# Optimization experiments

Measured on AMD Instinct MI355X. Metric: run time of the kernel, lower is better.

## Reference

```python
import jax, jax.numpy as jnp
import numpy as np

D = 512
H = 8
HD = D // H
S = 2048
B = 4


def setup_inputs() -> dict:
    key = jax.random.key(0)
    ks = jax.random.split(key, 8)
    scale = 1.0 / np.sqrt(D)
    x = jax.random.normal(ks[0], (S, B, D), dtype=jnp.float32)
    head_mask = jax.random.normal(ks[1], (H, S, S), dtype=jnp.float32)
    value_gate = jax.random.uniform(ks[2], (1, B, 1), dtype=jnp.float32)
    # nn.MultiheadAttention parameters
    in_proj_w = jax.random.normal(ks[3], (3 * D, D), dtype=jnp.float32) * scale
    in_proj_b = jnp.zeros((3 * D,), dtype=jnp.float32)
    out_proj_w = jax.random.normal(ks[4], (D, D), dtype=jnp.float32) * scale
    out_proj_b = jnp.zeros((D,), dtype=jnp.float32)
    return {
        "x": x,
        "head_mask": head_mask,
        "value_gate": value_gate,
        "in_proj_w": in_proj_w,
        "in_proj_b": in_proj_b,
        "out_proj_w": out_proj_w,
        "out_proj_b": out_proj_b,
    }


def reference(x, head_mask, value_gate, in_proj_w, in_proj_b, out_proj_w, out_proj_b):
    # x: (S, B, D); head_mask: (H, S, S) additive; value_gate: (1, B, 1)
    v_in = x * value_gate  # value gating before projection
    wq, wk, wv = in_proj_w[:D], in_proj_w[D:2 * D], in_proj_w[2 * D:]
    bq, bk, bv = in_proj_b[:D], in_proj_b[D:2 * D], in_proj_b[2 * D:]
    q = x @ wq.T + bq            # (S, B, D)
    k = x @ wk.T + bk
    v = v_in @ wv.T + bv
    # split D into H heads of size HD (matches torch's view(S, B*H, HD))
    q = q.reshape(S, B, H, HD)
    k = k.reshape(S, B, H, HD)
    v = v.reshape(S, B, H, HD)
    scores = jnp.einsum('sbhd,tbhd->bhst', q, k) / np.sqrt(HD).astype(np.float32)
    scores = scores + head_mask[None]  # broadcast per-head mask over batch
    attn = jax.nn.softmax(scores, axis=-1)  # (B, H, S, S)
    out = jnp.einsum('bhst,tbhd->sbhd', attn, v).reshape(S, B, D)
    return out @ out_proj_w.T + out_proj_b
```

## Files before the change

kernel.cpp:

```cpp
#include <hip/hip_runtime.h>
#include <cstdint>
#include <cstddef>

typedef _Float16 half8 __attribute__((ext_vector_type(8)));
typedef _Float16 half4 __attribute__((ext_vector_type(4)));
typedef float f32x4 __attribute__((ext_vector_type(4)));

#define MFMA16(A,B,C) __builtin_amdgcn_mfma_f32_16x16x32_f16(A,B,C,0,0,0)

__device__ __forceinline__ void gll16(const _Float16* g, _Float16* l) {
    __builtin_amdgcn_global_load_lds(
        (const __attribute__((address_space(1))) void*)g,
        (__attribute__((address_space(3))) void*)l, 16, 0, 0);
}

__global__ __launch_bounds__(256) void cvt_f16(
    const float* __restrict__ X, const float* __restrict__ Wi, const float* __restrict__ Wo,
    _Float16* __restrict__ Xh, _Float16* __restrict__ Wih, _Float16* __restrict__ Woh)
{
    const size_t i8 = ((size_t)blockIdx.x * 256 + threadIdx.x) * 8;
    const size_t NX = (size_t)4194304, NWI = 786432;
    const float* src; _Float16* dst; size_t off;
    if (i8 < NX) { src = X; dst = Xh; off = i8; }
    else if (i8 < NX + NWI) { src = Wi; dst = Wih; off = i8 - NX; }
    else { src = Wo; dst = Woh; off = i8 - NX - NWI; }
    f32x4 v0 = *(const f32x4*)(src + off);
    f32x4 v1 = *(const f32x4*)(src + off + 4);
    half8 r;
    r[0]=(_Float16)v0[0]; r[1]=(_Float16)v0[1]; r[2]=(_Float16)v0[2]; r[3]=(_Float16)v0[3];
    r[4]=(_Float16)v1[0]; r[5]=(_Float16)v1[1]; r[6]=(_Float16)v1[2]; r[7]=(_Float16)v1[3];
    *(half8*)(dst + off) = r;
}

__global__ __launch_bounds__(256) void qkv_mfma(
    const _Float16* __restrict__ X, const _Float16* __restrict__ W,
    const float* __restrict__ bias, const float* __restrict__ gate,
    _Float16* __restrict__ Qo, _Float16* __restrict__ Ko, _Float16* __restrict__ Vt)
{
    __shared__ _Float16 As[128][72];
    __shared__ _Float16 Bs[64][72];
    const int tid = threadIdx.x;
    const int lane = tid & 63, wv = tid >> 6;
    const int l15 = lane & 15, g = lane >> 4;
    const int wr = wv >> 1, wc = wv & 1;
    const int j0 = blockIdx.x * 64, r0 = blockIdx.y * 128;
    f32x4 acc[4][2] = {};
    const int arow = tid >> 1, ahf = tid & 1;
    const int brow = tid >> 2, bc = tid & 3;
    for (int k0 = 0; k0 < 512; k0 += 64) {
        const _Float16* srca = X + (size_t)(r0 + arow) * 512 + k0 + ahf * 32;
#pragma unroll
        for (int c = 0; c < 4; ++c)
            *(half8*)&As[arow][ahf * 32 + c * 8] = *(const half8*)(srca + c * 8);
        const _Float16* srcb = W + (size_t)(j0 + brow) * 512 + k0 + bc * 16;
#pragma unroll
        for (int c = 0; c < 2; ++c)
            *(half8*)&Bs[brow][bc * 16 + c * 8] = *(const half8*)(srcb + c * 8);
        __syncthreads();
#pragma unroll
        for (int kt = 0; kt < 2; ++kt) {
            half8 bf0 = *(half8*)&Bs[32 * wc + l15][kt * 32 + g * 8];
            half8 bf1 = *(half8*)&Bs[32 * wc + 16 + l15][kt * 32 + g * 8];
#pragma unroll
            for (int ri = 0; ri < 4; ++ri) {
                half8 af = *(half8*)&As[64 * wr + 16 * ri + l15][kt * 32 + g * 8];
                acc[ri][0] = MFMA16(af, bf0, acc[ri][0]);
                acc[ri][1] = MFMA16(af, bf1, acc[ri][1]);
            }
        }
        __syncthreads();
    }
#pragma unroll
    for (int ri = 0; ri < 4; ++ri) {
#pragma unroll
        for (int cj = 0; cj < 2; ++cj) {
            const int col = j0 + 32 * wc + 16 * cj + l15;
            const int sec = col >> 9, hh = (col >> 6) & 7, d = col & 63;
            const float bv = bias[col];
#pragma unroll
            for (int r = 0; r < 4; ++r) {
                const int row = r0 + 64 * wr + 16 * ri + 4 * g + r;
                const int b = row & 3, s = row >> 2;
                const float v = acc[ri][cj][r];
                if (sec == 0)
                    Qo[((size_t)(b * 8 + hh) * 2048 + s) * 64 + d] = (_Float16)((v + bv) * 0.125f);
                else if (sec == 1)
                    Ko[((size_t)(b * 8 + hh) * 2048 + s) * 64 + d] = (_Float16)(v + bv);
                else {
                    const int ps = (s & ~31) | ((s & 12) << 1) | ((s & 16) >> 2) | (s & 3);
                    Vt[((size_t)(b * 8 + hh) * 64 + d) * 2048 + ps] = (_Float16)(v * gate[b] + bv);
                }
            }
        }
    }
}

__global__ __launch_bounds__(128, 2) void attn_mfma(
    const _Float16* __restrict__ Q, const _Float16* __restrict__ K,
    const _Float16* __restrict__ V, const float* __restrict__ M,
    _Float16* __restrict__ P0, _Float16* __restrict__ P1, float* __restrict__ Lb)
{
    __shared__ _Float16 Kl[2][4096];
    __shared__ _Float16 Vl[2][4096];
    const int tid = threadIdx.x;
    const int lane = tid & 63, w = tid >> 6;
    const int l15 = lane & 15, g = lane >> 4;
    const int bsw = l15 & 7;
    const int bid = blockIdx.x;
    const int h = bid & 7, b = (bid >> 3) & 3, sg = (bid >> 5) & 15, kvh = bid >> 9;
    const int s0 = sg * 128 + w * 64;
    const size_t bh = (size_t)b * 8 + h;
    const _Float16* Qp = Q + bh * 2048 * 64;
    const _Float16* Kp = K + bh * 2048 * 64 + (size_t)kvh * 1024 * 64;
    const _Float16* Vp = V + bh * 64 * 2048 + kvh * 1024;
    const float* Mp = M + (size_t)h * 2048 * 2048 + kvh * 1024;

    half8 qf[4][2];
#pragma unroll
    for (int qj = 0; qj < 4; ++qj)
#pragma unroll
        for (int dh = 0; dh < 2; ++dh)
            qf[qj][dh] = *(const half8*)(Qp + (size_t)(s0 + 16 * qj + l15) * 64 + dh * 32 + g * 8);

    const int grow = lane >> 3, gcb = lane & 7;

    if (w == 0) {
#pragma unroll
        for (int c = 0; c < 8; ++c) {
            const int r = c * 8 + grow;
            gll16(Kp + (size_t)r * 64 + ((gcb ^ (r & 7)) * 8), &Kl[0][c * 512]);
        }
    } else {
#pragma unroll
        for (int c = 0; c < 8; ++c) {
            const int d = c * 8 + grow;
            gll16(Vp + (size_t)d * 2048 + ((gcb ^ (d & 7)) * 8), &Vl[0][c * 512]);
        }
    }
    f32x4 mc0[2][4], mc1[2][4];
#pragma unroll
    for (int mi = 0; mi < 2; ++mi)
#pragma unroll
        for (int qj = 0; qj < 4; ++qj)
            mc0[mi][qj] = *(const f32x4*)(Mp + (size_t)(s0 + 16 * qj + l15) * 2048 + 16 * mi + 4 * g);

    f32x4 O[4][4] = {};
    float l[4] = {0.f, 0.f, 0.f, 0.f};
    __syncthreads();

    for (int tl = 0; tl < 16; ++tl) {
        const int cur = tl & 1;
        const int t0 = tl * 64;
        const int tn = ((tl + 1) & 15) * 64;
        if (tl < 15) {
            if (w == 0) {
#pragma unroll
                for (int c = 0; c < 8; ++c) {
                    const int r = c * 8 + grow;
                    gll16(Kp + (size_t)(t0 + 64 + r) * 64 + ((gcb ^ (r & 7)) * 8),
                          &Kl[cur ^ 1][c * 512]);
                }
            } else {
#pragma unroll
                for (int c = 0; c < 8; ++c) {
                    const int d = c * 8 + grow;
                    gll16(Vp + (size_t)d * 2048 + t0 + 64 + ((gcb ^ (d & 7)) * 8),
                          &Vl[cur ^ 1][c * 512]);
                }
            }
        }

        f32x4 St[2][4];
        __builtin_amdgcn_s_setprio(1);
#pragma unroll
        for (int mi = 0; mi < 2; ++mi) {
            const int row = 16 * mi + l15;
            half8 kf0 = *(half8*)&Kl[cur][row * 64 + ((g) ^ bsw) * 8];
            half8 kf1 = *(half8*)&Kl[cur][row * 64 + ((4 + g) ^ bsw) * 8];
#pragma unroll
            for (int qj = 0; qj < 4; ++qj) {
                St[mi][qj] = MFMA16(kf0, qf[qj][0], mc0[mi][qj]);
                St[mi][qj] = MFMA16(kf1, qf[qj][1], St[mi][qj]);
            }
        }
        __builtin_amdgcn_s_setprio(0);
#pragma unroll
        for (int mi = 0; mi < 2; ++mi)
#pragma unroll
            for (int qj = 0; qj < 4; ++qj)
                mc1[mi][qj] = *(const f32x4*)(Mp + (size_t)(s0 + 16 * qj + l15) * 2048 + t0 + 16 * (2 + mi) + 4 * g);
        half8 pfA[4];
#pragma unroll
        for (int qj = 0; qj < 4; ++qj) {
            float e00 = __expf(St[0][qj][0]), e01 = __expf(St[0][qj][1]);
            float e02 = __expf(St[0][qj][2]), e03 = __expf(St[0][qj][3]);
            float e10 = __expf(St[1][qj][0]), e11 = __expf(St[1][qj][1]);
            float e12 = __expf(St[1][qj][2]), e13 = __expf(St[1][qj][3]);
            l[qj] += ((e00 + e01) + (e02 + e03)) + ((e10 + e11) + (e12 + e13));
            half8 p;
            p[0] = (_Float16)e00; p[1] = (_Float16)e01; p[2] = (_Float16)e02; p[3] = (_Float16)e03;
            p[4] = (_Float16)e10; p[5] = (_Float16)e11; p[6] = (_Float16)e12; p[7] = (_Float16)e13;
            pfA[qj] = p;
        }
        __builtin_amdgcn_s_setprio(1);
#pragma unroll
        for (int di = 0; di < 4; ++di) {
            const int vrow = 16 * di + l15;
            half8 vf = *(half8*)&Vl[cur][vrow * 64 + ((g) ^ bsw) * 8];
#pragma unroll
            for (int qj = 0; qj < 4; ++qj)
                O[di][qj] = MFMA16(vf, pfA[qj], O[di][qj]);
        }
        __builtin_amdgcn_s_setprio(0);

        __builtin_amdgcn_s_setprio(1);
#pragma unroll
        for (int mi = 0; mi < 2; ++mi) {
            const int row = 16 * (2 + mi) + l15;
            half8 kf0 = *(half8*)&Kl[cur][row * 64 + ((g) ^ bsw) * 8];
            half8 kf1 = *(half8*)&Kl[cur][row * 64 + ((4 + g) ^ bsw) * 8];
#pragma unroll
            for (int qj = 0; qj < 4; ++qj) {
                St[mi][qj] = MFMA16(kf0, qf[qj][0], mc1[mi][qj]);
                St[mi][qj] = MFMA16(kf1, qf[qj][1], St[mi][qj]);
            }
        }
        __builtin_amdgcn_s_setprio(0);
#pragma unroll
        for (int mi = 0; mi < 2; ++mi)
#pragma unroll
            for (int qj = 0; qj < 4; ++qj)
                mc0[mi][qj] = *(const f32x4*)(Mp + (size_t)(s0 + 16 * qj + l15) * 2048 + tn + 16 * mi + 4 * g);
        half8 pfB[4];
#pragma unroll
        for (int qj = 0; qj < 4; ++qj) {
            float e00 = __expf(St[0][qj][0]), e01 = __expf(St[0][qj][1]);
            float e02 = __expf(St[0][qj][2]), e03 = __expf(St[0][qj][3]);
            float e10 = __expf(St[1][qj][0]), e11 = __expf(St[1][qj][1]);
            float e12 = __expf(St[1][qj][2]), e13 = __expf(St[1][qj][3]);
            l[qj] += ((e00 + e01) + (e02 + e03)) + ((e10 + e11) + (e12 + e13));
            half8 p;
            p[0] = (_Float16)e00; p[1] = (_Float16)e01; p[2] = (_Float16)e02; p[3] = (_Float16)e03;
            p[4] = (_Float16)e10; p[5] = (_Float16)e11; p[6] = (_Float16)e12; p[7] = (_Float16)e13;
            pfB[qj] = p;
        }
        __builtin_amdgcn_s_setprio(1);
#pragma unroll
        for (int di = 0; di < 4; ++di) {
            const int vrow = 16 * di + l15;
            half8 vf = *(half8*)&Vl[cur][vrow * 64 + ((4 + g) ^ bsw) * 8];
#pragma unroll
            for (int qj = 0; qj < 4; ++qj)
                O[di][qj] = MFMA16(vf, pfB[qj], O[di][qj]);
        }
        __builtin_amdgcn_s_setprio(0);

        __syncthreads();
    }

    _Float16* P = kvh ? P1 : P0;
#pragma unroll
    for (int qj = 0; qj < 4; ++qj) {
        float lt = l[qj];
        lt += __shfl_xor(lt, 16);
        lt += __shfl_xor(lt, 32);
        const float inv = 1.0f / lt;
        const int q = s0 + 16 * qj + l15;
        const int r = q * 4 + b;
        _Float16* dst = P + (size_t)r * 512 + h * 64;
#pragma unroll
        for (int di = 0; di < 4; ++di) {
            half4 o;
            o[0] = (_Float16)(O[di][qj][0] * inv); o[1] = (_Float16)(O[di][qj][1] * inv);
            o[2] = (_Float16)(O[di][qj][2] * inv); o[3] = (_Float16)(O[di][qj][3] * inv);
            *(half4*)(dst + 16 * di + 4 * g) = o;
        }
        if (g == 0)
            Lb[(size_t)kvh * 65536 + r * 8 + h] = lt;
    }
}

__global__ __launch_bounds__(256) void merge_attn(
    const _Float16* __restrict__ P0, const _Float16* __restrict__ P1,
    const float* __restrict__ Lb, _Float16* __restrict__ AO)
{
    const size_t e = ((size_t)blockIdx.x * 256 + threadIdx.x) * 8;
    const int r = (int)(e >> 9);
    const int h = (int)((e & 511) >> 6);
    const int li = r * 8 + h;
    const float l0 = Lb[li], l1 = Lb[65536 + li];
    const float inv = 1.0f / (l0 + l1);
    const float a0 = l0 * inv, a1 = l1 * inv;
    half8 x0 = *(const half8*)(P0 + e);
    half8 x1 = *(const half8*)(P1 + e);
    half8 o;
#pragma unroll
    for (int i = 0; i < 8; ++i)
        o[i] = (_Float16)(a0 * (float)x0[i] + a1 * (float)x1[i]);
    *(half8*)(AO + e) = o;
}

__global__ __launch_bounds__(256) void oproj_mfma(
    const _Float16* __restrict__ A, const _Float16* __restrict__ W,
    const float* __restrict__ bias, float* __restrict__ Out)
{
    __shared__ _Float16 As[128][72];
    __shared__ _Float16 Bs[64][72];
    const int tid = threadIdx.x;
    const int lane = tid & 63, wv = tid >> 6;
    const int l15 = lane & 15, g = lane >> 4;
    const int wr = wv >> 1, wc = wv & 1;
    const int j0 = blockIdx.x * 64, r0 = blockIdx.y * 128;
    f32x4 acc[4][2] = {};
    const int arow = tid >> 1, ahf = tid & 1;
    const int brow = tid >> 2, bc = tid & 3;
    for (int k0 = 0; k0 < 512; k0 += 64) {
        const _Float16* srca = A + (size_t)(r0 + arow) * 512 + k0 + ahf * 32;
#pragma unroll
        for (int c = 0; c < 4; ++c)
            *(half8*)&As[arow][ahf * 32 + c * 8] = *(const half8*)(srca + c * 8);
        const _Float16* srcb = W + (size_t)(j0 + brow) * 512 + k0 + bc * 16;
#pragma unroll
        for (int c = 0; c < 2; ++c)
            *(half8*)&Bs[brow][bc * 16 + c * 8] = *(const half8*)(srcb + c * 8);
        __syncthreads();
#pragma unroll
        for (int kt = 0; kt < 2; ++kt) {
            half8 bf0 = *(half8*)&Bs[32 * wc + l15][kt * 32 + g * 8];
            half8 bf1 = *(half8*)&Bs[32 * wc + 16 + l15][kt * 32 + g * 8];
#pragma unroll
            for (int ri = 0; ri < 4; ++ri) {
                half8 af = *(half8*)&As[64 * wr + 16 * ri + l15][kt * 32 + g * 8];
                acc[ri][0] = MFMA16(af, bf0, acc[ri][0]);
                acc[ri][1] = MFMA16(af, bf1, acc[ri][1]);
            }
        }
        __syncthreads();
    }
#pragma unroll
    for (int ri = 0; ri < 4; ++ri) {
#pragma unroll
        for (int cj = 0; cj < 2; ++cj) {
            const int col = j0 + 32 * wc + 16 * cj + l15;
            const float bv = bias[col];
#pragma unroll
            for (int r = 0; r < 4; ++r) {
                const int row = r0 + 64 * wr + 16 * ri + 4 * g + r;
                Out[(size_t)row * 512 + col] = acc[ri][cj][r] + bv;
            }
        }
    }
}

extern "C" void kernel_launch(void* const* d_in, const int* in_sizes, int n_in,
                              void* d_out, int out_size, void* d_ws, size_t ws_size,
                              hipStream_t stream)
{
    (void)in_sizes; (void)n_in; (void)out_size; (void)ws_size;
    const float* X    = (const float*)d_in[0];
    const float* Mask = (const float*)d_in[1];
    const float* gate = (const float*)d_in[2];
    const float* Wi   = (const float*)d_in[3];
    const float* bi   = (const float*)d_in[4];
    const float* Wo   = (const float*)d_in[5];
    const float* bo   = (const float*)d_in[6];
    _Float16* ws = (_Float16*)d_ws;
    const size_t plane = (size_t)4 * 8 * 2048 * 64;
    _Float16* Qh  = ws;
    _Float16* Kh  = ws + plane;
    _Float16* Vt  = ws + 2 * plane;
    _Float16* AO  = ws + 3 * plane;
    _Float16* Xh  = ws + 4 * plane;
    _Float16* Wih = ws + 5 * plane;
    _Float16* Woh = ws + 5 * plane + 786432;
    _Float16* P0  = Xh;
    _Float16* P1  = ws + 5 * plane + 1048576;
    float*    Lb  = (float*)(ws + 5 * plane + 1048576 + plane);

    cvt_f16<<<dim3(2560), 256, 0, stream>>>(X, Wi, Wo, Xh, Wih, Woh);
    qkv_mfma<<<dim3(24, 64), 256, 0, stream>>>(Xh, Wih, bi, gate, Qh, Kh, Vt);
    attn_mfma<<<dim3(1024), 128, 0, stream>>>(Qh, Kh, Vt, Mask, P0, P1, Lb);
    merge_attn<<<dim3(2048), 256, 0, stream>>>(P0, P1, Lb, AO);
    oproj_mfma<<<dim3(8, 64), 256, 0, stream>>>(AO, Woh, bo, (float*)d_out);
}
```

Measured before the change: 139.9 us.

## Share head-mask tile across batch in attention and split KV into four chunks

```diff
diff --git a/kernel.cpp b/kernel.cpp
--- a/kernel.cpp
+++ b/kernel.cpp
@@ -95,54 +95,63 @@
     }
 }
 
-__global__ __launch_bounds__(128, 2) void attn_mfma(
+__global__ __launch_bounds__(256) void attn_mfma(
     const _Float16* __restrict__ Q, const _Float16* __restrict__ K,
     const _Float16* __restrict__ V, const float* __restrict__ M,
-    _Float16* __restrict__ P0, _Float16* __restrict__ P1, float* __restrict__ Lb)
-{
-    __shared__ _Float16 Kl[2][4096];
-    __shared__ _Float16 Vl[2][4096];
+    _Float16* __restrict__ P0, _Float16* __restrict__ P1,
+    _Float16* __restrict__ P2, _Float16* __restrict__ P3, float* __restrict__ Lb)
+{
+    __shared__ _Float16 Kl[2][4][32][64];
+    __shared__ _Float16 Vl[2][4][64][32];
     const int tid = threadIdx.x;
     const int lane = tid & 63, w = tid >> 6;
     const int l15 = lane & 15, g = lane >> 4;
-    const int bsw = l15 & 7;
     const int bid = blockIdx.x;
-    const int h = bid & 7, b = (bid >> 3) & 3, sg = (bid >> 5) & 15, kvh = bid >> 9;
-    const int s0 = sg * 128 + w * 64;
-    const size_t bh = (size_t)b * 8 + h;
-    const _Float16* Qp = Q + bh * 2048 * 64;
-    const _Float16* Kp = K + bh * 2048 * 64 + (size_t)kvh * 1024 * 64;
-    const _Float16* Vp = V + bh * 64 * 2048 + kvh * 1024;
-    const float* Mp = M + (size_t)h * 2048 * 2048 + kvh * 1024;
+    const int kvh = bid & 3, h = (bid >> 2) & 7, qg = bid >> 5;
+    const int q0 = qg * 64 + w * 16;
+    const _Float16* Qp[4]; const _Float16* Kp[4]; const _Float16* Vp[4];
+#pragma unroll
+    for (int b = 0; b < 4; ++b) {
+        const size_t bh = (size_t)b * 8 + h;
+        Qp[b] = Q + bh * 2048 * 64;
+        Kp[b] = K + (bh * 2048 + (size_t)kvh * 512) * 64;
+        Vp[b] = V + bh * 64 * 2048 + kvh * 512;
+    }
+    const float* Mp = M + (size_t)h * 2048 * 2048 + kvh * 512;
 
     half8 qf[4][2];
 #pragma unroll
-    for (int qj = 0; qj < 4; ++qj)
+    for (int b = 0; b < 4; ++b)
 #pragma unroll
         for (int dh = 0; dh < 2; ++dh)
-            qf[qj][dh] = *(const half8*)(Qp + (size_t)(s0 + 16 * qj + l15) * 64 + dh * 32 + g * 8);
-
-    const int grow = lane >> 3, gcb = lane & 7;
-
-    if (w == 0) {
-#pragma unroll
-        for (int c = 0; c < 8; ++c) {
-            const int r = c * 8 + grow;
-            gll16(Kp + (size_t)r * 64 + ((gcb ^ (r & 7)) * 8), &Kl[0][c * 512]);
-        }
+            qf[b][dh] = *(const half8*)(Qp[b] + (size_t)(q0 + l15) * 64 + dh * 32 + g * 8);
+
+    const bool stK = (w < 2);
+    const int b0 = (w & 1) * 2;
+    const int krow = lane >> 3, kblk = lane & 7;
+    const int vrow = lane >> 2, vblk = lane & 3;
+    const int ksw = (kblk ^ (krow & 7)) * 8;
+    const int vsw = (vblk ^ ((vrow >> 1) & 3)) * 8;
+
+    if (stK) {
+#pragma unroll
+        for (int bb = 0; bb < 2; ++bb)
+#pragma unroll
+            for (int c = 0; c < 4; ++c)
+                gll16(Kp[b0 + bb] + (size_t)(c * 8 + krow) * 64 + ksw,
+                      &Kl[0][b0 + bb][c * 8][0]);
     } else {
 #pragma unroll
-        for (int c = 0; c < 8; ++c) {
-            const int d = c * 8 + grow;
-            gll16(Vp + (size_t)d * 2048 + ((gcb ^ (d & 7)) * 8), &Vl[0][c * 512]);
-        }
-    }
-    f32x4 mc0[2][4], mc1[2][4];
+        for (int bb = 0; bb < 2; ++bb)
+#pragma unroll
+            for (int c = 0; c < 4; ++c)
+                gll16(Vp[b0 + bb] + (size_t)(c * 16 + vrow) * 2048 + vsw,
+                      &Vl[0][b0 + bb][c * 16][0]);
+    }
+    f32x4 mc[2];
 #pragma unroll
     for (int mi = 0; mi < 2; ++mi)
-#pragma unroll
-        for (int qj = 0; qj < 4; ++qj)
-            mc0[mi][qj] = *(const f32x4*)(Mp + (size_t)(s0 + 16 * qj + l15) * 2048 + 16 * mi + 4 * g);
+        mc[mi] = *(const f32x4*)(Mp + (size_t)(q0 + l15) * 2048 + 16 * mi + 4 * g);
 
     f32x4 O[4][4] = {};
     float l[4] = {0.f, 0.f, 0.f, 0.f};
@@ -150,129 +159,90 @@
 
     for (int tl = 0; tl < 16; ++tl) {
         const int cur = tl & 1;
-        const int t0 = tl * 64;
-        const int tn = ((tl + 1) & 15) * 64;
+        const int t0 = tl * 32;
         if (tl < 15) {
-            if (w == 0) {
-#pragma unroll
-                for (int c = 0; c < 8; ++c) {
-                    const int r = c * 8 + grow;
-                    gll16(Kp + (size_t)(t0 + 64 + r) * 64 + ((gcb ^ (r & 7)) * 8),
-                          &Kl[cur ^ 1][c * 512]);
-                }
+            const int tg = t0 + 32;
+            if (stK) {
+#pragma unroll
+                for (int bb = 0; bb < 2; ++bb)
+#pragma unroll
+                    for (int c = 0; c < 4; ++c)
+                        gll16(Kp[b0 + bb] + (size_t)(tg + c * 8 + krow) * 64 + ksw,
+                              &Kl[cur ^ 1][b0 + bb][c * 8][0]);
             } else {
 #pragma unroll
-                for (int c = 0; c < 8; ++c) {
-                    const int d = c * 8 + grow;
-                    gll16(Vp + (size_t)d * 2048 + t0 + 64 + ((gcb ^ (d & 7)) * 8),
-                          &Vl[cur ^ 1][c * 512]);
-                }
+                for (int bb = 0; bb < 2; ++bb)
+#pragma unroll
+                    for (int c = 0; c < 4; ++c)
+                        gll16(Vp[b0 + bb] + (size_t)(c * 16 + vrow) * 2048 + tg + vsw,
+                              &Vl[cur ^ 1][b0 + bb][c * 16][0]);
             }
         }
 
         f32x4 St[2][4];
         __builtin_amdgcn_s_setprio(1);
 #pragma unroll
-        for (int mi = 0; mi < 2; ++mi) {
-            const int row = 16 * mi + l15;
-            half8 kf0 = *(half8*)&Kl[cur][row * 64 + ((g) ^ bsw) * 8];
-            half8 kf1 = *(half8*)&Kl[cur][row * 64 + ((4 + g) ^ bsw) * 8];
-#pragma unroll
-            for (int qj = 0; qj < 4; ++qj) {
-                St[mi][qj] = MFMA16(kf0, qf[qj][0], mc0[mi][qj]);
-                St[mi][qj] = MFMA16(kf1, qf[qj][1], St[mi][qj]);
+        for (int b = 0; b < 4; ++b) {
+#pragma unroll
+            for (int mi = 0; mi < 2; ++mi) {
+                const int row = 16 * mi + l15;
+                half8 kf0 = *(half8*)&Kl[cur][b][row][((g) ^ (l15 & 7)) * 8];
+                half8 kf1 = *(half8*)&Kl[cur][b][row][((4 + g) ^ (l15 & 7)) * 8];
+                St[mi][b] = MFMA16(kf0, qf[b][0], mc[mi]);
+                St[mi][b] = MFMA16(kf1, qf[b][1], St[mi][b]);
             }
         }
         __builtin_amdgcn_s_setprio(0);
-#pragma unroll
-        for (int mi = 0; mi < 2; ++mi)
-#pragma unroll
-            for (int qj = 0; qj < 4; ++qj)
-                mc1[mi][qj] = *(const f32x4*)(Mp + (size_t)(s0 + 16 * qj + l15) * 2048 + t0 + 16 * (2 + mi) + 4 * g);
-        half8 pfA[4];
-#pragma unroll
-        for (int qj = 0; qj < 4; ++qj) {
-            float e00 = __expf(St[0][qj][0]), e01 = __expf(St[0][qj][1]);
-            float e02 = __expf(St[0][qj][2]), e03 = __expf(St[0][qj][3]);
-            float e10 = __expf(St[1][qj][0]), e11 = __expf(St[1][qj][1]);
-            float e12 = __expf(St[1][qj][2]), e13 = __expf(St[1][qj][3]);
-            l[qj] += ((e00 + e01) + (e02 + e03)) + ((e10 + e11) + (e12 + e13));
+
+        const int tn = ((tl + 1) & 15) * 32;
+        f32x4 mn0 = *(const f32x4*)(Mp + (size_t)(q0 + l15) * 2048 + tn + 4 * g);
+        f32x4 mn1 = *(const f32x4*)(Mp + (size_t)(q0 + l15) * 2048 + tn + 16 + 4 * g);
+
+        half8 pf[4];
+#pragma unroll
+        for (int b = 0; b < 4; ++b) {
+            float e0 = __expf(St[0][b][0]), e1 = __expf(St[0][b][1]);
+            float e2 = __expf(St[0][b][2]), e3 = __expf(St[0][b][3]);
+            float e4 = __expf(St[1][b][0]), e5 = __expf(St[1][b][1]);
+            float e6 = __expf(St[1][b][2]), e7 = __expf(St[1][b][3]);
+            l[b] += ((e0 + e1) + (e2 + e3)) + ((e4 + e5) + (e6 + e7));
             half8 p;
-            p[0] = (_Float16)e00; p[1] = (_Float16)e01; p[2] = (_Float16)e02; p[3] = (_Float16)e03;
-            p[4] = (_Float16)e10; p[5] = (_Float16)e11; p[6] = (_Float16)e12; p[7] = (_Float16)e13;
-            pfA[qj] = p;
-        }
+            p[0] = (_Float16)e0; p[1] = (_Float16)e1; p[2] = (_Float16)e2; p[3] = (_Float16)e3;
+            p[4] = (_Float16)e4; p[5] = (_Float16)e5; p[6] = (_Float16)e6; p[7] = (_Float16)e7;
+            pf[b] = p;
+        }
+
         __builtin_amdgcn_s_setprio(1);
 #pragma unroll
-        for (int di = 0; di < 4; ++di) {
-            const int vrow = 16 * di + l15;
-            half8 vf = *(half8*)&Vl[cur][vrow * 64 + ((g) ^ bsw) * 8];
-#pragma unroll
-            for (int qj = 0; qj < 4; ++qj)
-                O[di][qj] = MFMA16(vf, pfA[qj], O[di][qj]);
+        for (int b = 0; b < 4; ++b) {
+#pragma unroll
+            for (int di = 0; di < 4; ++di) {
+                const int row = 16 * di + l15;
+                half8 vf = *(half8*)&Vl[cur][b][row][(g ^ ((l15 >> 1) & 3)) * 8];
+                O[di][b] = MFMA16(vf, pf[b], O[di][b]);
+            }
         }
         __builtin_amdgcn_s_setprio(0);
 
-        __builtin_amdgcn_s_setprio(1);
-#pragma unroll
-        for (int mi = 0; mi < 2; ++mi) {
-            const int row = 16 * (2 + mi) + l15;
-            half8 kf0 = *(half8*)&Kl[cur][row * 64 + ((g) ^ bsw) * 8];
-            half8 kf1 = *(half8*)&Kl[cur][row * 64 + ((4 + g) ^ bsw) * 8];
-#pragma unroll
-            for (int qj = 0; qj < 4; ++qj) {
-                St[mi][qj] = MFMA16(kf0, qf[qj][0], mc1[mi][qj]);
-                St[mi][qj] = MFMA16(kf1, qf[qj][1], St[mi][qj]);
-            }
-        }
-        __builtin_amdgcn_s_setprio(0);
-#pragma unroll
-        for (int mi = 0; mi < 2; ++mi)
-#pragma unroll
-            for (int qj = 0; qj < 4; ++qj)
-                mc0[mi][qj] = *(const f32x4*)(Mp + (size_t)(s0 + 16 * qj + l15) * 2048 + tn + 16 * mi + 4 * g);
-        half8 pfB[4];
-#pragma unroll
-        for (int qj = 0; qj < 4; ++qj) {
-            float e00 = __expf(St[0][qj][0]), e01 = __expf(St[0][qj][1]);
-            float e02 = __expf(St[0][qj][2]), e03 = __expf(St[0][qj][3]);
-            float e10 = __expf(St[1][qj][0]), e11 = __expf(St[1][qj][1]);
-            float e12 = __expf(St[1][qj][2]), e13 = __expf(St[1][qj][3]);
-            l[qj] += ((e00 + e01) + (e02 + e03)) + ((e10 + e11) + (e12 + e13));
-            half8 p;
-            p[0] = (_Float16)e00; p[1] = (_Float16)e01; p[2] = (_Float16)e02; p[3] = (_Float16)e03;
-            p[4] = (_Float16)e10; p[5] = (_Float16)e11; p[6] = (_Float16)e12; p[7] = (_Float16)e13;
-            pfB[qj] = p;
-        }
-        __builtin_amdgcn_s_setprio(1);
-#pragma unroll
-        for (int di = 0; di < 4; ++di) {
-            const int vrow = 16 * di + l15;
-            half8 vf = *(half8*)&Vl[cur][vrow * 64 + ((4 + g) ^ bsw) * 8];
-#pragma unroll
-            for (int qj = 0; qj < 4; ++qj)
-                O[di][qj] = MFMA16(vf, pfB[qj], O[di][qj]);
-        }
-        __builtin_amdgcn_s_setprio(0);
-
-        __syncthreads();
-    }
-
-    _Float16* P = kvh ? P1 : P0;
-#pragma unroll
-    for (int qj = 0; qj < 4; ++qj) {
-        float lt = l[qj];
+        mc[0] = mn0; mc[1] = mn1;
+        __syncthreads();
+    }
+
+#pragma unroll
+    for (int b = 0; b < 4; ++b) {
+        float lt = l[b];
         lt += __shfl_xor(lt, 16);
         lt += __shfl_xor(lt, 32);
         const float inv = 1.0f / lt;
-        const int q = s0 + 16 * qj + l15;
+        const int q = q0 + l15;
         const int r = q * 4 + b;
+        _Float16* P = (kvh == 0) ? P0 : (kvh == 1) ? P1 : (kvh == 2) ? P2 : P3;
         _Float16* dst = P + (size_t)r * 512 + h * 64;
 #pragma unroll
         for (int di = 0; di < 4; ++di) {
             half4 o;
-            o[0] = (_Float16)(O[di][qj][0] * inv); o[1] = (_Float16)(O[di][qj][1] * inv);
-            o[2] = (_Float16)(O[di][qj][2] * inv); o[3] = (_Float16)(O[di][qj][3] * inv);
+            o[0] = (_Float16)(O[di][b][0] * inv); o[1] = (_Float16)(O[di][b][1] * inv);
+            o[2] = (_Float16)(O[di][b][2] * inv); o[3] = (_Float16)(O[di][b][3] * inv);
             *(half4*)(dst + 16 * di + 4 * g) = o;
         }
         if (g == 0)
@@ -282,6 +252,7 @@
 
 __global__ __launch_bounds__(256) void merge_attn(
     const _Float16* __restrict__ P0, const _Float16* __restrict__ P1,
+    const _Float16* __restrict__ P2, const _Float16* __restrict__ P3,
     const float* __restrict__ Lb, _Float16* __restrict__ AO)
 {
     const size_t e = ((size_t)blockIdx.x * 256 + threadIdx.x) * 8;
@@ -289,14 +260,18 @@
     const int h = (int)((e & 511) >> 6);
     const int li = r * 8 + h;
     const float l0 = Lb[li], l1 = Lb[65536 + li];
-    const float inv = 1.0f / (l0 + l1);
-    const float a0 = l0 * inv, a1 = l1 * inv;
+    const float l2 = Lb[131072 + li], l3 = Lb[196608 + li];
+    const float inv = 1.0f / (l0 + l1 + l2 + l3);
+    const float a0 = l0 * inv, a1 = l1 * inv, a2 = l2 * inv, a3 = l3 * inv;
     half8 x0 = *(const half8*)(P0 + e);
     half8 x1 = *(const half8*)(P1 + e);
+    half8 x2 = *(const half8*)(P2 + e);
+    half8 x3 = *(const half8*)(P3 + e);
     half8 o;
 #pragma unroll
     for (int i = 0; i < 8; ++i)
-        o[i] = (_Float16)(a0 * (float)x0[i] + a1 * (float)x1[i]);
+        o[i] = (_Float16)(a0 * (float)x0[i] + a1 * (float)x1[i]
+                        + a2 * (float)x2[i] + a3 * (float)x3[i]);
     *(half8*)(AO + e) = o;
 }
 
@@ -375,11 +350,13 @@
     _Float16* Woh = ws + 5 * plane + 786432;
     _Float16* P0  = Xh;
     _Float16* P1  = ws + 5 * plane + 1048576;
-    float*    Lb  = (float*)(ws + 5 * plane + 1048576 + plane);
+    _Float16* P2  = P1 + plane;
+    _Float16* P3  = P2 + plane;
+    float*    Lb  = (float*)(P3 + plane);
 
     cvt_f16<<<dim3(2560), 256, 0, stream>>>(X, Wi, Wo, Xh, Wih, Woh);
     qkv_mfma<<<dim3(24, 64), 256, 0, stream>>>(Xh, Wih, bi, gate, Qh, Kh, Vt);
-    attn_mfma<<<dim3(1024), 128, 0, stream>>>(Qh, Kh, Vt, Mask, P0, P1, Lb);
-    merge_attn<<<dim3(2048), 256, 0, stream>>>(P0, P1, Lb, AO);
+    attn_mfma<<<dim3(1024), 256, 0, stream>>>(Qh, Kh, Vt, Mask, P0, P1, P2, P3, Lb);
+    merge_attn<<<dim3(2048), 256, 0, stream>>>(P0, P1, P2, P3, Lb, AO);
     oproj_mfma<<<dim3(8, 64), 256, 0, stream>>>(AO, Woh, bo, (float*)d_out);
 }
```

New measurement: 134.1 us. 4.2% less time.
